# Kernel optimization log

Measured on AMD Instinct MI355X. Metric: run time of the kernel, lower is better.

The kernel has to match this reference:

```python
import jax, jax.numpy as jnp
import numpy as np

NEG_SLOPE = 0.2
NUM_GRAPHS = 64


def _gat_layer(x, src, dst, W, att_src, att_dst, bias, concat):
    # x: [N, Fin]; W: [Fin, H*C]; att_*: [H, C]; bias: [H*C] or [C]
    N = x.shape[0]
    H, C = att_src.shape
    h = (x @ W).reshape(N, H, C)                      # per-head projections
    a_src = jnp.sum(h * att_src, axis=-1)             # [N, H]
    a_dst = jnp.sum(h * att_dst, axis=-1)             # [N, H]
    e = jax.nn.leaky_relu(a_src[src] + a_dst[dst], NEG_SLOPE)  # [E, H]
    # segment softmax over incoming edges per destination node
    m = jnp.full((N, H), -jnp.inf, dtype=e.dtype).at[dst].max(e)
    p = jnp.exp(e - m[dst])                           # [E, H]
    denom = jnp.zeros((N, H), dtype=e.dtype).at[dst].add(p)
    alpha = p / denom[dst]                            # [E, H]
    msg = h[src] * alpha[:, :, None]                  # [E, H, C]
    out = jnp.zeros((N, H, C), dtype=h.dtype).at[dst].add(msg)
    out = out.reshape(N, H * C) if concat else out.mean(axis=1)
    return out + bias


def _with_self_loops(edge_index, n):
    loop = jnp.arange(n, dtype=edge_index.dtype)
    src = jnp.concatenate([edge_index[0], loop])
    dst = jnp.concatenate([edge_index[1], loop])
    return src, dst


def setup_inputs() -> dict:
    key = jax.random.key(0)
    ks = jax.random.split(key, 12)
    N, E, Fin, C, H, A = 50000, 800000, 128, 64, 4, 32
    HC = H * C
    x = jax.random.normal(ks[0], (N, Fin), dtype=jnp.float32)
    edge_index = jax.random.randint(ks[1], (2, E), 0, N, dtype=jnp.int64)
    batch = jnp.sort(jax.random.randint(ks[2], (N,), 0, NUM_GRAPHS, dtype=jnp.int64))
    s1 = 1.0 / np.sqrt(Fin)
    s2 = 1.0 / np.sqrt(HC)
    return {
        "x": x,
        "edge_index": edge_index,
        "batch": batch,
        "num_wires": 8,
        "num_terminals": 8,
        "W1": jax.random.normal(ks[3], (Fin, HC), dtype=jnp.float32) * s1,
        "att_src1": jax.random.normal(ks[4], (H, C), dtype=jnp.float32) * s1,
        "att_dst1": jax.random.normal(ks[5], (H, C), dtype=jnp.float32) * s1,
        "b1": jnp.zeros((HC,), dtype=jnp.float32),
        "W2": jax.random.normal(ks[6], (HC, HC), dtype=jnp.float32) * s2,
        "att_src2": jax.random.normal(ks[7], (H, C), dtype=jnp.float32) * s2,
        "att_dst2": jax.random.normal(ks[8], (H, C), dtype=jnp.float32) * s2,
        "b2": jnp.zeros((C,), dtype=jnp.float32),
        "Wa": jax.random.normal(ks[9], (C, A), dtype=jnp.float32) * (1.0 / np.sqrt(C)),
        "ba": jnp.zeros((A,), dtype=jnp.float32),
    }


def reference(x, edge_index, batch, num_wires, num_terminals,
              W1, att_src1, att_dst1, b1, W2, att_src2, att_dst2, b2, Wa, ba):
    N = x.shape[0]
    src, dst = _with_self_loops(edge_index, N)
    h = jax.nn.elu(_gat_layer(x, src, dst, W1, att_src1, att_dst1, b1, concat=True))
    h = jax.nn.elu(_gat_layer(h, src, dst, W2, att_src2, att_dst2, b2, concat=False))
    # global mean pool per graph
    sums = jax.ops.segment_sum(h, batch, num_segments=NUM_GRAPHS)
    cnts = jax.ops.segment_sum(jnp.ones((N,), dtype=h.dtype), batch, num_segments=NUM_GRAPHS)
    pooled = sums / jnp.maximum(cnts, 1.0)[:, None]   # [G, C]
    return pooled @ Wa + ba                            # [G, num_actions]
```

## Files before the change

kernel.cpp:

```cpp
#include <hip/hip_runtime.h>
#include <hip/hip_bf16.h>
#include <cstdint>
#include <cstddef>

#define FIN      128
#define HGAT_H   4
#define HGAT_C   64
#define HGAT_HC  256
#define NGRAPHS  64
#define NACT     32
#define LOG2E    1.4426950408889634f
#define CNT_BLOCKS 128

typedef unsigned int   uint32;
typedef unsigned short ushort_t;

using short8 = __attribute__((ext_vector_type(8))) short;
using u16x8  = __attribute__((ext_vector_type(8))) ushort_t;
using f32x4  = __attribute__((ext_vector_type(4))) float;
using f32x2  = __attribute__((ext_vector_type(2))) float;

__device__ __forceinline__ float bf2f(ushort_t u) {
    return __uint_as_float(((uint32)u) << 16);
}
__device__ __forceinline__ float bflo(uint32 q) {
    return __uint_as_float(q << 16);
}
__device__ __forceinline__ float bfhi(uint32 q) {
    return __uint_as_float(q & 0xFFFF0000u);
}
__device__ __forceinline__ ushort_t f2bf(float f) {
    __hip_bfloat16 h = __float2bfloat16(f);
    return *reinterpret_cast<ushort_t*>(&h);
}

__device__ __forceinline__ void att_fold_one(
    const float* __restrict__ W, const float* __restrict__ as,
    const float* __restrict__ ad, ushort_t* __restrict__ attBt,
    int K, int idx)
{
    const int k = idx >> 3, j = idx & 7;
    const int h = j >> 1;
    const float* av = (j & 1) ? ad : as;
    float s = 0.f;
#pragma unroll 8
    for (int c = 0; c < HGAT_C; ++c)
        s += W[(size_t)k * HGAT_HC + h * 64 + c] * av[h * 64 + c];
    const ushort_t hi = f2bf(s);
    const float    lo = s - bf2f(hi);
    attBt[(size_t)j * K + k]       = hi;
    attBt[(size_t)(j + 8) * K + k] = f2bf(lo);
}

__global__ __launch_bounds__(256) void bucket_count_prep_kernel(
    const int* __restrict__ ei, int* __restrict__ bhist,
    const float* __restrict__ W1, const float* __restrict__ W2,
    const float* __restrict__ as1, const float* __restrict__ ad1,
    const float* __restrict__ as2, const float* __restrict__ ad2,
    ushort_t* __restrict__ Wt1, ushort_t* __restrict__ Wt2,
    ushort_t* __restrict__ attBt1, ushort_t* __restrict__ attBt2, int E)
{
    const int t = threadIdx.x;
    if (blockIdx.x < CNT_BLOCKS) {
        __shared__ int hist[256];
        hist[t] = 0;
        __syncthreads();
        const int chunk = (E + CNT_BLOCKS - 1) / CNT_BLOCKS;
        const int lo = blockIdx.x * chunk;
        const int hi = min(lo + chunk, E);
        for (int e = lo + t; e < hi; e += 256)
            atomicAdd(&hist[ei[E + e] >> 8], 1);
        __syncthreads();
        bhist[blockIdx.x * 256 + t] = hist[t];
        return;
    }
    const int idx = (blockIdx.x - CNT_BLOCKS) * 256 + t;
    const int n1 = FIN * HGAT_HC;
    const int n2 = HGAT_HC * HGAT_HC;
    if (idx < n1) {
        const int k = idx >> 8, c = idx & 255;
        Wt1[(size_t)c * FIN + k] = f2bf(W1[idx]);
    } else if (idx < n1 + n2) {
        const int j = idx - n1;
        const int k = j >> 8, c = j & 255;
        Wt2[(size_t)c * HGAT_HC + k] = f2bf(W2[j]);
    } else if (idx < n1 + n2 + FIN * 8) {
        att_fold_one(W1, as1, ad1, attBt1, FIN, idx - n1 - n2);
    } else if (idx < n1 + n2 + (FIN + HGAT_HC) * 8) {
        att_fold_one(W2, as2, ad2, attBt2, HGAT_HC, idx - n1 - n2 - FIN * 8);
    }
}

__global__ __launch_bounds__(256) void bucket_scan_kernel(
    const int* __restrict__ bhist, int* __restrict__ boff,
    int* __restrict__ bcur)
{
    __shared__ int sm[256];
    const int t = threadIdx.x;
    int v = 0;
    for (int j = 0; j < CNT_BLOCKS; ++j) v += bhist[j * 256 + t];
    sm[t] = v;
    __syncthreads();
#pragma unroll
    for (int off = 1; off < 256; off <<= 1) {
        const int u = (t >= off) ? sm[t - off] : 0;
        __syncthreads();
        sm[t] += u;
        __syncthreads();
    }
    const int ex = sm[t] - v;
    boff[t] = ex;
    bcur[t] = ex;
    if (t == 255) boff[256] = sm[255];
}

__device__ __forceinline__ void scatter_body(
    const int* __restrict__ ei, int* __restrict__ bcur,
    int2* __restrict__ staging, int E, int blk)
{
    __shared__ int hist[256];
    __shared__ int base[256];
    __shared__ int cur[256];
    const int t = threadIdx.x;
    hist[t] = 0;
    __syncthreads();

    const int chunk = 4096;
    const int lo = blk * chunk;
    const int hi = min(lo + chunk, E);

    for (int e = lo + t; e < hi; e += 256)
        atomicAdd(&hist[ei[E + e] >> 8], 1);
    __syncthreads();
    if (hist[t] > 0) base[t] = atomicAdd(&bcur[t], hist[t]);
    cur[t] = 0;
    __syncthreads();

    for (int e = lo + t; e < hi; e += 256) {
        const int s = ei[e];
        const int d = ei[E + e];
        const int b = d >> 8;
        const int r = atomicAdd(&cur[b], 1);
        staging[base[b] + r] = make_int2(s, d);
    }
}

__global__ __launch_bounds__(256) void bucket_fill_kernel(
    const int2* __restrict__ staging, const int* __restrict__ boff,
    int* __restrict__ rowptr, int* __restrict__ colsrc, int N, int E)
{
    __shared__ int deg[256];
    __shared__ int ssc[256];
    __shared__ int cur[256];
    const int t  = threadIdx.x;
    const int b  = blockIdx.x;
    const int lo = boff[b];
    const int hi = boff[b + 1];

    deg[t] = 0;
    __syncthreads();
    for (int e = lo + t; e < hi; e += 256)
        atomicAdd(&deg[staging[e].y & 255], 1);
    __syncthreads();

    const int v = deg[t];
    ssc[t] = v;
    __syncthreads();
#pragma unroll
    for (int off = 1; off < 256; off <<= 1) {
        const int u = (t >= off) ? ssc[t - off] : 0;
        __syncthreads();
        ssc[t] += u;
        __syncthreads();
    }
    const int pre  = ssc[t] - v;
    const int node = b * 256 + t;
    if (node < N) rowptr[node] = lo + pre;
    cur[t] = lo + pre;
    if (b == 0 && t == 0) rowptr[N] = E;
    __syncthreads();

    for (int e = lo + t; e < hi; e += 256) {
        const int2 sd = staging[e];
        const int pos = atomicAdd(&cur[sd.y & 255], 1);
        colsrc[pos] = sd.x;
    }
}

template <int K, bool AF32>
__device__ __forceinline__ void gemm_body(
    const void* __restrict__ Av, const ushort_t* __restrict__ Bt,
    const ushort_t* __restrict__ attBt, ushort_t* __restrict__ Cb,
    float* __restrict__ a_src, float* __restrict__ a_dst, int M, int blk)
{
    constexpr int KK   = K / 32;
    constexpr int NPF  = K / 32;
    constexpr int BSTR = K + 8;
    constexpr int CSTR = 72;
    __shared__ ushort_t Bs[64 * BSTR];
    __shared__ ushort_t AttS[16 * BSTR];
    __shared__ ushort_t Cs[64 * CSTR];

    const int t  = threadIdx.x;
    const int w  = t >> 6;
    const int l  = t & 63;
    const int lg = l >> 4;
    const int lr = l & 15;
    const int rowbase = blk * 64 + w * 16;

    const int srow  = t & 63;
    const int cbase = (t >> 6) * (K / 4);

    short8 af[KK];
    {
        const int arow = rowbase + lr;
        const int gr   = arow < M ? arow : M - 1;
        if (AF32) {
            const float* Ap = (const float*)Av + (size_t)gr * K;
#pragma unroll
            for (int kk = 0; kk < KK; ++kk) {
                const float4 v0 = *reinterpret_cast<const float4*>(Ap + kk * 32 + lg * 8);
                const float4 v1 = *reinterpret_cast<const float4*>(Ap + kk * 32 + lg * 8 + 4);
                short8 s;
                s[0] = (short)f2bf(v0.x); s[1] = (short)f2bf(v0.y);
                s[2] = (short)f2bf(v0.z); s[3] = (short)f2bf(v0.w);
                s[4] = (short)f2bf(v1.x); s[5] = (short)f2bf(v1.y);
                s[6] = (short)f2bf(v1.z); s[7] = (short)f2bf(v1.w);
                af[kk] = s;
            }
        } else {
            const ushort_t* Ap = (const ushort_t*)Av + (size_t)gr * K;
#pragma unroll
            for (int kk = 0; kk < KK; ++kk)
                af[kk] = *reinterpret_cast<const short8*>(Ap + kk * 32 + lg * 8);
        }
    }

    {
        const int r  = t & 15;
        const int cb = (t >> 4) * (K / 16);
        const ushort_t* src = attBt + (size_t)r * K + cb;
        ushort_t*       dst = &AttS[r * BSTR + cb];
#pragma unroll
        for (int j = 0; j < K / 128; ++j)
            *reinterpret_cast<u16x8*>(dst + j * 8) =
                *reinterpret_cast<const u16x8*>(src + j * 8);
    }
    {
        const ushort_t* src = Bt + (size_t)srow * K + cbase;
        ushort_t*       dst = &Bs[srow * BSTR + cbase];
#pragma unroll
        for (int j = 0; j < NPF; ++j)
            *reinterpret_cast<u16x8*>(dst + j * 8) =
                *reinterpret_cast<const u16x8*>(src + j * 8);
    }
    __syncthreads();

    {
        f32x4 aacc = {0.f, 0.f, 0.f, 0.f};
#pragma unroll
        for (int kk = 0; kk < KK; ++kk) {
            const short8 bfr = *reinterpret_cast<const short8*>(
                &AttS[lr * BSTR + kk * 32 + lg * 8]);
            aacc = __builtin_amdgcn_mfma_f32_16x16x32_bf16(af[kk], bfr, aacc, 0, 0, 0);
        }
#pragma unroll
        for (int reg = 0; reg < 4; ++reg) {
            const int gm = rowbase + lg * 4 + reg;
            const float v = aacc[reg] + __shfl_xor(aacc[reg], 8);
            if (lr < 8 && gm < M) {
                const int hh = lr >> 1;
                if (lr & 1) a_dst[gm * 4 + hh] = v * LOG2E;
                else        a_src[gm * 4 + hh] = v * LOG2E;
            }
        }
    }

    u16x8 pf[NPF];
#pragma unroll
    for (int head = 0; head < HGAT_H; ++head) {
        if (head < HGAT_H - 1) {
            const ushort_t* src =
                Bt + ((size_t)(head + 1) * 64 + srow) * K + cbase;
#pragma unroll
            for (int j = 0; j < NPF; ++j)
                pf[j] = *reinterpret_cast<const u16x8*>(src + j * 8);
        }

        f32x4 acc[4];
#pragma unroll
        for (int ct = 0; ct < 4; ++ct) acc[ct] = {0.f, 0.f, 0.f, 0.f};

#pragma unroll
        for (int kk = 0; kk < KK; ++kk) {
            short8 bfr[4];
#pragma unroll
            for (int ct = 0; ct < 4; ++ct)
                bfr[ct] = *reinterpret_cast<const short8*>(
                    &Bs[(ct * 16 + lr) * BSTR + kk * 32 + lg * 8]);
#pragma unroll
            for (int ct = 0; ct < 4; ++ct)
                acc[ct] = __builtin_amdgcn_mfma_f32_16x16x32_bf16(
                    af[kk], bfr[ct], acc[ct], 0, 0, 0);
        }

#pragma unroll
        for (int reg = 0; reg < 4; ++reg) {
            const int r = w * 16 + lg * 4 + reg;
#pragma unroll
            for (int ct = 0; ct < 4; ++ct)
                Cs[r * CSTR + ct * 16 + lr] = f2bf(acc[ct][reg]);
        }
        __syncthreads();

        const int n0 = head * 64;
        {
            const int cc = (t & 7) * 8;
#pragma unroll
            for (int it = 0; it < 2; ++it) {
                const int r  = (t >> 3) + it * 32;
                const int gm = blk * 64 + r;
                if (gm < M) {
                    const u16x8 val = *reinterpret_cast<const u16x8*>(&Cs[r * CSTR + cc]);
                    *reinterpret_cast<u16x8*>(&Cb[(size_t)gm * HGAT_HC + n0 + cc]) = val;
                }
            }
        }

        if (head < HGAT_H - 1) {
            ushort_t* dst = &Bs[srow * BSTR + cbase];
#pragma unroll
            for (int j = 0; j < NPF; ++j)
                *reinterpret_cast<u16x8*>(dst + j * 8) = pf[j];
        }
        __syncthreads();
    }
}

__global__ __launch_bounds__(256) void scatter_gemm1_kernel(
    const int* __restrict__ ei, int* __restrict__ bcur,
    int2* __restrict__ staging, int E, int SB,
    const float* __restrict__ x, const ushort_t* __restrict__ Wt1,
    const ushort_t* __restrict__ attBt1, ushort_t* __restrict__ hb,
    float* __restrict__ a_src, float* __restrict__ a_dst, int M)
{
    if ((int)blockIdx.x < SB) {
        scatter_body(ei, bcur, staging, E, blockIdx.x);
        return;
    }
    gemm_body<FIN, true>(x, Wt1, attBt1, hb, a_src, a_dst, M,
                         blockIdx.x - SB);
}

__global__ __launch_bounds__(256) void gemm2_kernel(
    const ushort_t* __restrict__ A, const ushort_t* __restrict__ Wt2,
    const ushort_t* __restrict__ attBt2, ushort_t* __restrict__ hb,
    float* __restrict__ a_src, float* __restrict__ a_dst, int M)
{
    gemm_body<HGAT_HC, false>(A, Wt2, attBt2, hb, a_src, a_dst, M, blockIdx.x);
}

template <int MODE>
__global__ __launch_bounds__(256) void aggregate_csr_kernel(
    const int* __restrict__ rowptr, const int* __restrict__ colsrc,
    const ushort_t* __restrict__ hb, const float* __restrict__ a_src,
    const float* __restrict__ a_dst, const float* __restrict__ bias,
    ushort_t* __restrict__ out, int N)
{
    const int wave = (blockIdx.x * 256 + threadIdx.x) >> 6;
    const int lane = threadIdx.x & 63;
    const int half = lane >> 5;
    const int hl   = lane & 31;
    const int d    = wave * 2 + half;
    if (d >= N) return;

    const int c0 = hl * 8;
    const int h  = hl >> 3;
    const float ad = a_dst[d * 4 + h];

    f32x2 a01 = {0.f, 0.f}, a23 = {0.f, 0.f}, a45 = {0.f, 0.f}, a67 = {0.f, 0.f};
    float den = 0.f;

    const int beg = rowptr[d], end = rowptr[d + 1];
    int i = beg;
    for (; i + 4 <= end; i += 4) {
        int   sv[4];
        float av[4];
        uint4 qv[4];
#pragma unroll
        for (int j = 0; j < 4; ++j) sv[j] = colsrc[i + j];
#pragma unroll
        for (int j = 0; j < 4; ++j) av[j] = a_src[sv[j] * 4 + h];
#pragma unroll
        for (int j = 0; j < 4; ++j)
            qv[j] = *reinterpret_cast<const uint4*>(&hb[(size_t)sv[j] * HGAT_HC + c0]);
#pragma unroll
        for (int j = 0; j < 4; ++j) {
            float ee = av[j] + ad;
            ee = fmaxf(ee, 0.2f * ee);
            const float wgt = __builtin_amdgcn_exp2f(ee);
            const f32x2 w2 = {wgt, wgt};
            a01 += w2 * f32x2{bflo(qv[j].x), bfhi(qv[j].x)};
            a23 += w2 * f32x2{bflo(qv[j].y), bfhi(qv[j].y)};
            a45 += w2 * f32x2{bflo(qv[j].z), bfhi(qv[j].z)};
            a67 += w2 * f32x2{bflo(qv[j].w), bfhi(qv[j].w)};
            den += wgt;
        }
    }
    for (; i < end; ++i) {
        const int s = colsrc[i];
        float ee = a_src[s * 4 + h] + ad;
        ee = fmaxf(ee, 0.2f * ee);
        const float wgt = __builtin_amdgcn_exp2f(ee);
        const uint4 q = *reinterpret_cast<const uint4*>(&hb[(size_t)s * HGAT_HC + c0]);
        const f32x2 w2 = {wgt, wgt};
        a01 += w2 * f32x2{bflo(q.x), bfhi(q.x)};
        a23 += w2 * f32x2{bflo(q.y), bfhi(q.y)};
        a45 += w2 * f32x2{bflo(q.z), bfhi(q.z)};
        a67 += w2 * f32x2{bflo(q.w), bfhi(q.w)};
        den += wgt;
    }
    {
        float ee = a_src[d * 4 + h] + ad;
        ee = fmaxf(ee, 0.2f * ee);
        const float wgt = __builtin_amdgcn_exp2f(ee);
        const uint4 q = *reinterpret_cast<const uint4*>(&hb[(size_t)d * HGAT_HC + c0]);
        const f32x2 w2 = {wgt, wgt};
        a01 += w2 * f32x2{bflo(q.x), bfhi(q.x)};
        a23 += w2 * f32x2{bflo(q.y), bfhi(q.y)};
        a45 += w2 * f32x2{bflo(q.z), bfhi(q.z)};
        a67 += w2 * f32x2{bflo(q.w), bfhi(q.w)};
        den += wgt;
    }

    const float inv = 1.0f / den;
    float v[8] = {a01.x * inv, a01.y * inv, a23.x * inv, a23.y * inv,
                  a45.x * inv, a45.y * inv, a67.x * inv, a67.y * inv};

    if (MODE == 0) {
        const float4 b0 = *reinterpret_cast<const float4*>(&bias[c0]);
        const float4 b1 = *reinterpret_cast<const float4*>(&bias[c0 + 4]);
        v[0] += b0.x; v[1] += b0.y; v[2] += b0.z; v[3] += b0.w;
        v[4] += b1.x; v[5] += b1.y; v[6] += b1.z; v[7] += b1.w;
        u16x8 u;
#pragma unroll
        for (int j = 0; j < 8; ++j) {
            const float r = v[j] > 0.f ? v[j] : expm1f(v[j]);
            u[j] = f2bf(r);
        }
        *reinterpret_cast<u16x8*>(&out[(size_t)d * HGAT_HC + c0]) = u;
    } else {
#pragma unroll
        for (int j = 0; j < 8; ++j) {
            v[j] += __shfl_xor(v[j], 8);
            v[j] += __shfl_xor(v[j], 16);
        }
        if (hl < 8) {
            const int c = hl * 8;
            const float4 b0 = *reinterpret_cast<const float4*>(&bias[c]);
            const float4 b1 = *reinterpret_cast<const float4*>(&bias[c + 4]);
            const float bb[8] = {b0.x, b0.y, b0.z, b0.w, b1.x, b1.y, b1.z, b1.w};
            u16x8 u;
#pragma unroll
            for (int j = 0; j < 8; ++j) {
                float r = 0.25f * v[j] + bb[j];
                r = r > 0.f ? r : expm1f(r);
                u[j] = f2bf(r);
            }
            *reinterpret_cast<u16x8*>(&out[(size_t)d * HGAT_C + c]) = u;
        }
    }
}

__device__ __forceinline__ int lower_bound_batch(
    const int* __restrict__ batch, int N, int key)
{
    int lo = 0, hi = N;
    while (lo < hi) {
        const int mid = (lo + hi) >> 1;
        if (batch[mid] < key) lo = mid + 1; else hi = mid;
    }
    return lo;
}

__global__ __launch_bounds__(256) void pool_partial_kernel(
    const ushort_t* __restrict__ hfin, const int* __restrict__ batch,
    float* __restrict__ partial, int N)
{
    const int g   = blockIdx.x >> 3;
    const int s   = blockIdx.x & 7;
    const int t   = threadIdx.x;
    const int c   = t & 63;
    const int sub = t >> 6;

    const int beg = lower_bound_batch(batch, N, g);
    const int end = lower_bound_batch(batch, N, g + 1);
    const int len = end - beg;
    const int sl  = (len + 7) >> 3;
    const int sb  = beg + s * sl;
    const int se  = sb + sl < end ? sb + sl : end;

    float acc = 0.f;
    for (int n = sb + sub; n < se; n += 4)
        acc += bf2f(hfin[(size_t)n * HGAT_C + c]);

    __shared__ float sm[256];
    sm[t] = acc;
    __syncthreads();
    if (sub == 0)
        partial[(size_t)(g * 8 + s) * HGAT_C + c] =
            sm[c] + sm[64 + c] + sm[128 + c] + sm[192 + c];
}

__global__ __launch_bounds__(64) void pool_final_fused_kernel(
    const float* __restrict__ partial, const int* __restrict__ batch,
    const float* __restrict__ Wa, const float* __restrict__ ba,
    float* __restrict__ out, int N)
{
    const int g = blockIdx.x;
    const int c = threadIdx.x;
    const int beg = lower_bound_batch(batch, N, g);
    const int end = lower_bound_batch(batch, N, g + 1);
    float s = 0.f;
#pragma unroll
    for (int k = 0; k < 8; ++k)
        s += partial[(size_t)(g * 8 + k) * HGAT_C + c];
    s /= fmaxf((float)(end - beg), 1.0f);

    __shared__ float pr[HGAT_C];
    pr[c] = s;
    __syncthreads();
    if (c < NACT) {
        float o = ba[c];
#pragma unroll
        for (int cc = 0; cc < HGAT_C; ++cc)
            o += pr[cc] * Wa[cc * NACT + c];
        out[g * NACT + c] = o;
    }
}

extern "C" void kernel_launch(void* const* d_in, const int* in_sizes, int n_in,
                              void* d_out, int out_size, void* d_ws, size_t ws_size,
                              hipStream_t stream)
{
    const float* x     = (const float*)d_in[0];
    const int*   ei    = (const int*)d_in[1];
    const int*   batch = (const int*)d_in[2];
    const float* W1    = (const float*)d_in[5];
    const float* as1   = (const float*)d_in[6];
    const float* ad1   = (const float*)d_in[7];
    const float* b1    = (const float*)d_in[8];
    const float* W2    = (const float*)d_in[9];
    const float* as2   = (const float*)d_in[10];
    const float* ad2   = (const float*)d_in[11];
    const float* b2    = (const float*)d_in[12];
    const float* Wa    = (const float*)d_in[13];
    const float* ba    = (const float*)d_in[14];

    const int N = in_sizes[0] / FIN;
    const int E = in_sizes[1] / 2;

    char* ws = (char*)d_ws;
    size_t off = 0;
    auto alloc = [&](size_t bytes) -> void* {
        void* p = ws + off;
        off += (bytes + 255) & ~(size_t)255;
        return p;
    };
    ushort_t* hb      = (ushort_t*)alloc((size_t)N * HGAT_HC * 2);
    ushort_t* hpost   = (ushort_t*)alloc((size_t)N * HGAT_HC * 2);
    ushort_t* Wt1     = (ushort_t*)alloc((size_t)FIN * HGAT_HC * 2);
    ushort_t* Wt2     = (ushort_t*)alloc((size_t)HGAT_HC * HGAT_HC * 2);
    ushort_t* attBt1  = (ushort_t*)alloc((size_t)16 * FIN * 2);
    ushort_t* attBt2  = (ushort_t*)alloc((size_t)16 * HGAT_HC * 2);
    float*    a_src   = (float*)alloc((size_t)N * 4 * 4);
    float*    a_dst   = (float*)alloc((size_t)N * 4 * 4);
    int*      rowptr  = (int*)alloc((size_t)(N + 1) * 4);
    int*      colsrc  = (int*)alloc((size_t)E * 4);
    int2*     staging = (int2*)alloc((size_t)E * 8);
    int*      bhist   = (int*)alloc((size_t)CNT_BLOCKS * 256 * 4);
    int*      boff    = (int*)alloc(257 * 4);
    int*      bcur    = (int*)alloc(256 * 4);
    float*    partial = (float*)alloc((size_t)NGRAPHS * 8 * HGAT_C * 4);
    ushort_t* hfin    = hpost;
    (void)ws_size; (void)n_in; (void)out_size;

    const int gemmBlocks = (N + 63) / 64;
    const int aggBlocks  = (N + 7) / 8;
    const int NBKT       = (N + 255) >> 8;
    const int SB         = (E + 4095) / 4096;
    const int prepTot    = FIN * HGAT_HC + HGAT_HC * HGAT_HC + (FIN + HGAT_HC) * 8;
    const int prepBlocks = (prepTot + 255) / 256;

    bucket_count_prep_kernel<<<CNT_BLOCKS + prepBlocks, 256, 0, stream>>>(
        ei, bhist, W1, W2, as1, ad1, as2, ad2, Wt1, Wt2, attBt1, attBt2, E);

    bucket_scan_kernel<<<1, 256, 0, stream>>>(bhist, boff, bcur);

    scatter_gemm1_kernel<<<SB + gemmBlocks, 256, 0, stream>>>(
        ei, bcur, staging, E, SB, x, Wt1, attBt1, hb, a_src, a_dst, N);

    bucket_fill_kernel<<<NBKT, 256, 0, stream>>>(
        staging, boff, rowptr, colsrc, N, E);

    aggregate_csr_kernel<0><<<aggBlocks, 256, 0, stream>>>(
        rowptr, colsrc, hb, a_src, a_dst, b1, hpost, N);

    gemm2_kernel<<<gemmBlocks, 256, 0, stream>>>(
        hpost, Wt2, attBt2, hb, a_src, a_dst, N);
    aggregate_csr_kernel<1><<<aggBlocks, 256, 0, stream>>>(
        rowptr, colsrc, hb, a_src, a_dst, b2, hfin, N);

    pool_partial_kernel<<<NGRAPHS * 8, 256, 0, stream>>>(hfin, batch, partial, N);
    pool_final_fused_kernel<<<NGRAPHS, 64, 0, stream>>>(
        partial, batch, Wa, ba, (float*)d_out, N);
}
```

Measured before the change: 225.8 us.

## Store projections in channel-slice-major layout and aggregate per slice

GEMM outputs are written in a slice-major layout of 8 slices × N × 32 channels, so each slice's feature table is compact (3.2 MB) and more cache-friendly for the random gathers. Aggregation now launches one block per slice group: each wave handles one node, with 16 edges in parallel and 4 lanes covering 32 channels, followed by a shuffle reduction. The layer-2 head mean, bias and ELU move into the pool kernel, which now reads 256-wide rows. The trade-off is eight passes over the CSR indices and a_src, extra shuffle reductions, and idle lanes for low-degree nodes.

```diff
diff --git a/kernel.cpp b/kernel.cpp
--- a/kernel.cpp
+++ b/kernel.cpp
@@ -190,7 +190,7 @@
 template <int K, bool AF32>
 __device__ __forceinline__ void gemm_body(
     const void* __restrict__ Av, const ushort_t* __restrict__ Bt,
-    const ushort_t* __restrict__ attBt, ushort_t* __restrict__ Cb,
+    const ushort_t* __restrict__ attBt, ushort_t* __restrict__ CbT,
     float* __restrict__ a_src, float* __restrict__ a_dst, int M, int blk)
 {
     constexpr int KK   = K / 32;
@@ -313,16 +313,19 @@
         }
         __syncthreads();
 
-        const int n0 = head * 64;
         {
             const int cc = (t & 7) * 8;
+            const int ch = head * 64 + cc;
+            const int slice  = ch >> 5;
+            const int within = ch & 31;
 #pragma unroll
             for (int it = 0; it < 2; ++it) {
                 const int r  = (t >> 3) + it * 32;
                 const int gm = blk * 64 + r;
                 if (gm < M) {
                     const u16x8 val = *reinterpret_cast<const u16x8*>(&Cs[r * CSTR + cc]);
-                    *reinterpret_cast<u16x8*>(&Cb[(size_t)gm * HGAT_HC + n0 + cc]) = val;
+                    *reinterpret_cast<u16x8*>(
+                        &CbT[((size_t)slice * M + gm) * 32 + within]) = val;
                 }
             }
         }
@@ -341,134 +344,101 @@
     const int* __restrict__ ei, int* __restrict__ bcur,
     int2* __restrict__ staging, int E, int SB,
     const float* __restrict__ x, const ushort_t* __restrict__ Wt1,
-    const ushort_t* __restrict__ attBt1, ushort_t* __restrict__ hb,
+    const ushort_t* __restrict__ attBt1, ushort_t* __restrict__ hbT,
     float* __restrict__ a_src, float* __restrict__ a_dst, int M)
 {
     if ((int)blockIdx.x < SB) {
         scatter_body(ei, bcur, staging, E, blockIdx.x);
         return;
     }
-    gemm_body<FIN, true>(x, Wt1, attBt1, hb, a_src, a_dst, M,
+    gemm_body<FIN, true>(x, Wt1, attBt1, hbT, a_src, a_dst, M,
                          blockIdx.x - SB);
 }
 
 __global__ __launch_bounds__(256) void gemm2_kernel(
     const ushort_t* __restrict__ A, const ushort_t* __restrict__ Wt2,
-    const ushort_t* __restrict__ attBt2, ushort_t* __restrict__ hb,
+    const ushort_t* __restrict__ attBt2, ushort_t* __restrict__ hbT,
     float* __restrict__ a_src, float* __restrict__ a_dst, int M)
 {
-    gemm_body<HGAT_HC, false>(A, Wt2, attBt2, hb, a_src, a_dst, M, blockIdx.x);
+    gemm_body<HGAT_HC, false>(A, Wt2, attBt2, hbT, a_src, a_dst, M, blockIdx.x);
 }
 
 template <int MODE>
-__global__ __launch_bounds__(256) void aggregate_csr_kernel(
+__global__ __launch_bounds__(256) void aggregate_slice_kernel(
     const int* __restrict__ rowptr, const int* __restrict__ colsrc,
-    const ushort_t* __restrict__ hb, const float* __restrict__ a_src,
+    const ushort_t* __restrict__ hbT, const float* __restrict__ a_src,
     const float* __restrict__ a_dst, const float* __restrict__ bias,
     ushort_t* __restrict__ out, int N)
 {
-    const int wave = (blockIdx.x * 256 + threadIdx.x) >> 6;
+    const int slice = blockIdx.x & 7;
+    const int node  = (blockIdx.x >> 3) * 4 + (threadIdx.x >> 6);
+    if (node >= N) return;
     const int lane = threadIdx.x & 63;
-    const int half = lane >> 5;
-    const int hl   = lane & 31;
-    const int d    = wave * 2 + half;
-    if (d >= N) return;
-
-    const int c0 = hl * 8;
-    const int h  = hl >> 3;
-    const float ad = a_dst[d * 4 + h];
-
-    f32x2 a01 = {0.f, 0.f}, a23 = {0.f, 0.f}, a45 = {0.f, 0.f}, a67 = {0.f, 0.f};
-    float den = 0.f;
-
-    const int beg = rowptr[d], end = rowptr[d + 1];
-    int i = beg;
-    for (; i + 4 <= end; i += 4) {
-        int   sv[4];
-        float av[4];
-        uint4 qv[4];
-#pragma unroll
-        for (int j = 0; j < 4; ++j) sv[j] = colsrc[i + j];
-#pragma unroll
-        for (int j = 0; j < 4; ++j) av[j] = a_src[sv[j] * 4 + h];
-#pragma unroll
-        for (int j = 0; j < 4; ++j)
-            qv[j] = *reinterpret_cast<const uint4*>(&hb[(size_t)sv[j] * HGAT_HC + c0]);
-#pragma unroll
-        for (int j = 0; j < 4; ++j) {
-            float ee = av[j] + ad;
-            ee = fmaxf(ee, 0.2f * ee);
-            const float wgt = __builtin_amdgcn_exp2f(ee);
-            const f32x2 w2 = {wgt, wgt};
-            a01 += w2 * f32x2{bflo(qv[j].x), bfhi(qv[j].x)};
-            a23 += w2 * f32x2{bflo(qv[j].y), bfhi(qv[j].y)};
-            a45 += w2 * f32x2{bflo(qv[j].z), bfhi(qv[j].z)};
-            a67 += w2 * f32x2{bflo(qv[j].w), bfhi(qv[j].w)};
-            den += wgt;
-        }
-    }
-    for (; i < end; ++i) {
-        const int s = colsrc[i];
-        float ee = a_src[s * 4 + h] + ad;
+    const int slot = lane >> 2;
+    const int q    = lane & 3;
+    const int head = slice >> 1;
+    const ushort_t* hs = hbT + (size_t)slice * N * 32;
+    const float ad = a_dst[node * 4 + head];
+
+    float vv[9];
+#pragma unroll
+    for (int j = 0; j < 9; ++j) vv[j] = 0.f;
+
+    const int beg = rowptr[node], end = rowptr[node + 1];
+    for (int base = beg; base < end; base += 16) {
+        const int idx   = base + slot;
+        const bool ok   = idx < end;
+        const int s     = colsrc[ok ? idx : end - 1];
+        const float a   = a_src[s * 4 + head];
+        float ee = a + ad;
         ee = fmaxf(ee, 0.2f * ee);
-        const float wgt = __builtin_amdgcn_exp2f(ee);
-        const uint4 q = *reinterpret_cast<const uint4*>(&hb[(size_t)s * HGAT_HC + c0]);
-        const f32x2 w2 = {wgt, wgt};
-        a01 += w2 * f32x2{bflo(q.x), bfhi(q.x)};
-        a23 += w2 * f32x2{bflo(q.y), bfhi(q.y)};
-        a45 += w2 * f32x2{bflo(q.z), bfhi(q.z)};
-        a67 += w2 * f32x2{bflo(q.w), bfhi(q.w)};
-        den += wgt;
-    }
-    {
-        float ee = a_src[d * 4 + h] + ad;
+        const float w = ok ? __builtin_amdgcn_exp2f(ee) : 0.f;
+        const uint4 qv = *reinterpret_cast<const uint4*>(
+            hs + (size_t)s * 32 + q * 8);
+        vv[0] += w * bflo(qv.x); vv[1] += w * bfhi(qv.x);
+        vv[2] += w * bflo(qv.y); vv[3] += w * bfhi(qv.y);
+        vv[4] += w * bflo(qv.z); vv[5] += w * bfhi(qv.z);
+        vv[6] += w * bflo(qv.w); vv[7] += w * bfhi(qv.w);
+        vv[8] += w;
+    }
+    if (slot == 0) {
+        const float a = a_src[node * 4 + head];
+        float ee = a + ad;
         ee = fmaxf(ee, 0.2f * ee);
-        const float wgt = __builtin_amdgcn_exp2f(ee);
-        const uint4 q = *reinterpret_cast<const uint4*>(&hb[(size_t)d * HGAT_HC + c0]);
-        const f32x2 w2 = {wgt, wgt};
-        a01 += w2 * f32x2{bflo(q.x), bfhi(q.x)};
-        a23 += w2 * f32x2{bflo(q.y), bfhi(q.y)};
-        a45 += w2 * f32x2{bflo(q.z), bfhi(q.z)};
-        a67 += w2 * f32x2{bflo(q.w), bfhi(q.w)};
-        den += wgt;
-    }
-
-    const float inv = 1.0f / den;
-    float v[8] = {a01.x * inv, a01.y * inv, a23.x * inv, a23.y * inv,
-                  a45.x * inv, a45.y * inv, a67.x * inv, a67.y * inv};
-
-    if (MODE == 0) {
-        const float4 b0 = *reinterpret_cast<const float4*>(&bias[c0]);
-        const float4 b1 = *reinterpret_cast<const float4*>(&bias[c0 + 4]);
-        v[0] += b0.x; v[1] += b0.y; v[2] += b0.z; v[3] += b0.w;
-        v[4] += b1.x; v[5] += b1.y; v[6] += b1.z; v[7] += b1.w;
+        const float w = __builtin_amdgcn_exp2f(ee);
+        const uint4 qv = *reinterpret_cast<const uint4*>(
+            hs + (size_t)node * 32 + q * 8);
+        vv[0] += w * bflo(qv.x); vv[1] += w * bfhi(qv.x);
+        vv[2] += w * bflo(qv.y); vv[3] += w * bfhi(qv.y);
+        vv[4] += w * bflo(qv.z); vv[5] += w * bfhi(qv.z);
+        vv[6] += w * bflo(qv.w); vv[7] += w * bfhi(qv.w);
+        vv[8] += w;
+    }
+
+#pragma unroll
+    for (int off = 4; off < 64; off <<= 1)
+#pragma unroll
+        for (int j = 0; j < 9; ++j) vv[j] += __shfl_xor(vv[j], off);
+
+    if (slot == 0) {
+        const float inv = 1.0f / vv[8];
+        const int chb = slice * 32 + q * 8;
         u16x8 u;
-#pragma unroll
-        for (int j = 0; j < 8; ++j) {
-            const float r = v[j] > 0.f ? v[j] : expm1f(v[j]);
-            u[j] = f2bf(r);
-        }
-        *reinterpret_cast<u16x8*>(&out[(size_t)d * HGAT_HC + c0]) = u;
-    } else {
-#pragma unroll
-        for (int j = 0; j < 8; ++j) {
-            v[j] += __shfl_xor(v[j], 8);
-            v[j] += __shfl_xor(v[j], 16);
-        }
-        if (hl < 8) {
-            const int c = hl * 8;
-            const float4 b0 = *reinterpret_cast<const float4*>(&bias[c]);
-            const float4 b1 = *reinterpret_cast<const float4*>(&bias[c + 4]);
+        if (MODE == 0) {
+            const float4 b0 = *reinterpret_cast<const float4*>(&bias[chb]);
+            const float4 b1 = *reinterpret_cast<const float4*>(&bias[chb + 4]);
             const float bb[8] = {b0.x, b0.y, b0.z, b0.w, b1.x, b1.y, b1.z, b1.w};
-            u16x8 u;
 #pragma unroll
             for (int j = 0; j < 8; ++j) {
-                float r = 0.25f * v[j] + bb[j];
+                float r = vv[j] * inv + bb[j];
                 r = r > 0.f ? r : expm1f(r);
                 u[j] = f2bf(r);
             }
-            *reinterpret_cast<u16x8*>(&out[(size_t)d * HGAT_C + c]) = u;
-        }
+        } else {
+#pragma unroll
+            for (int j = 0; j < 8; ++j) u[j] = f2bf(vv[j] * inv);
+        }
+        *reinterpret_cast<u16x8*>(&out[(size_t)node * HGAT_HC + chb]) = u;
     }
 }
 
@@ -484,8 +454,8 @@
 }
 
 __global__ __launch_bounds__(256) void pool_partial_kernel(
-    const ushort_t* __restrict__ hfin, const int* __restrict__ batch,
-    float* __restrict__ partial, int N)
+    const ushort_t* __restrict__ hmid, const int* __restrict__ batch,
+    const float* __restrict__ b2, float* __restrict__ partial, int N)
 {
     const int g   = blockIdx.x >> 3;
     const int s   = blockIdx.x & 7;
@@ -500,9 +470,14 @@
     const int sb  = beg + s * sl;
     const int se  = sb + sl < end ? sb + sl : end;
 
+    const float bc = b2[c];
     float acc = 0.f;
-    for (int n = sb + sub; n < se; n += 4)
-        acc += bf2f(hfin[(size_t)n * HGAT_C + c]);
+    for (int n = sb + sub; n < se; n += 4) {
+        const ushort_t* row = hmid + (size_t)n * HGAT_HC;
+        float m = 0.25f * (bf2f(row[c]) + bf2f(row[64 + c]) +
+                           bf2f(row[128 + c]) + bf2f(row[192 + c])) + bc;
+        acc += m > 0.f ? m : expm1f(m);
+    }
 
     __shared__ float sm[256];
     sm[t] = acc;
@@ -567,7 +542,7 @@
         off += (bytes + 255) & ~(size_t)255;
         return p;
     };
-    ushort_t* hb      = (ushort_t*)alloc((size_t)N * HGAT_HC * 2);
+    ushort_t* hbT     = (ushort_t*)alloc((size_t)N * HGAT_HC * 2);
     ushort_t* hpost   = (ushort_t*)alloc((size_t)N * HGAT_HC * 2);
     ushort_t* Wt1     = (ushort_t*)alloc((size_t)FIN * HGAT_HC * 2);
     ushort_t* Wt2     = (ushort_t*)alloc((size_t)HGAT_HC * HGAT_HC * 2);
@@ -582,11 +557,11 @@
     int*      boff    = (int*)alloc(257 * 4);
     int*      bcur    = (int*)alloc(256 * 4);
     float*    partial = (float*)alloc((size_t)NGRAPHS * 8 * HGAT_C * 4);
-    ushort_t* hfin    = hpost;
+    ushort_t* hmid    = hpost;
     (void)ws_size; (void)n_in; (void)out_size;
 
     const int gemmBlocks = (N + 63) / 64;
-    const int aggBlocks  = (N + 7) / 8;
+    const int aggBlocks  = ((N + 3) / 4) * 8;
     const int NBKT       = (N + 255) >> 8;
     const int SB         = (E + 4095) / 4096;
     const int prepTot    = FIN * HGAT_HC + HGAT_HC * HGAT_HC + (FIN + HGAT_HC) * 8;
@@ -598,20 +573,21 @@
     bucket_scan_kernel<<<1, 256, 0, stream>>>(bhist, boff, bcur);
 
     scatter_gemm1_kernel<<<SB + gemmBlocks, 256, 0, stream>>>(
-        ei, bcur, staging, E, SB, x, Wt1, attBt1, hb, a_src, a_dst, N);
+        ei, bcur, staging, E, SB, x, Wt1, attBt1, hbT, a_src, a_dst, N);
 
     bucket_fill_kernel<<<NBKT, 256, 0, stream>>>(
         staging, boff, rowptr, colsrc, N, E);
 
-    aggregate_csr_kernel<0><<<aggBlocks, 256, 0, stream>>>(
-        rowptr, colsrc, hb, a_src, a_dst, b1, hpost, N);
+    aggregate_slice_kernel<0><<<aggBlocks, 256, 0, stream>>>(
+        rowptr, colsrc, hbT, a_src, a_dst, b1, hpost, N);
 
     gemm2_kernel<<<gemmBlocks, 256, 0, stream>>>(
-        hpost, Wt2, attBt2, hb, a_src, a_dst, N);
-    aggregate_csr_kernel<1><<<aggBlocks, 256, 0, stream>>>(
-        rowptr, colsrc, hb, a_src, a_dst, b2, hfin, N);
-
-    pool_partial_kernel<<<NGRAPHS * 8, 256, 0, stream>>>(hfin, batch, partial, N);
+        hpost, Wt2, attBt2, hbT, a_src, a_dst, N);
+    aggregate_slice_kernel<1><<<aggBlocks, 256, 0, stream>>>(
+        rowptr, colsrc, hbT, a_src, a_dst, b2, hmid, N);
+
+    pool_partial_kernel<<<NGRAPHS * 8, 256, 0, stream>>>(
+        hmid, batch, b2, partial, N);
     pool_final_fused_kernel<<<NGRAPHS, 64, 0, stream>>>(
         partial, batch, Wa, ba, (float*)d_out, N);
 }
```

Result: slower. 443.5 us (+96.4%).
